# Optimization experiments

Hardware: AMD Instinct MI355X
Metric: run time of the kernel (lower is better)

The kernel has to match this reference:

```python
import jax, jax.numpy as jnp
import numpy as np

T, H, E, I = 512, 2048, 8, 1024


def setup_inputs() -> dict:
    key = jax.random.key(0)
    k1, k2, k3, k4 = jax.random.split(key, 4)
    x = jax.random.normal(k1, (T, H), dtype=jnp.float32)
    router_logits = jax.random.normal(k2, (T, E), dtype=jnp.float32)
    # w13 stacks [gate; up] along the output dim: [E, 2I, H]
    w13_weight = jax.random.normal(k3, (E, 2 * I, H), dtype=jnp.float32) * (1.0 / np.sqrt(H))
    w2_weight = jax.random.normal(k4, (E, H, I), dtype=jnp.float32) * (1.0 / np.sqrt(I))
    return {"x": x, "router_logits": router_logits, "w13_weight": w13_weight,
            "w2_weight": w2_weight, "top_k": 2}


def reference(x, router_logits, w13_weight, w2_weight, top_k):
    t, h = x.shape
    e = router_logits.shape[-1]
    # select_experts: softmax -> top_k -> renormalize
    probs = jax.nn.softmax(router_logits.astype(jnp.float32), axis=-1)  # [T, E]
    topk_w, topk_ids = jax.lax.top_k(probs, top_k)                      # [T, K]
    topk_w = topk_w / jnp.sum(topk_w, axis=-1, keepdims=True)
    # dense combine weights [T, E]; zero for unselected experts
    combine = jnp.zeros((t, e), dtype=x.dtype).at[
        jnp.arange(t)[:, None], topk_ids
    ].add(topk_w.astype(x.dtype))
    # grouped expert SwiGLU MLP (computed densely over experts, masked by combine)
    gu = jnp.einsum('th,enh->ten', x, w13_weight)   # [T, E, 2I]
    i = gu.shape[-1] // 2
    gate, up = gu[..., :i], gu[..., i:]
    act = jax.nn.silu(gate) * up                    # [T, E, I]
    y = jnp.einsum('tei,ehi->teh', act, w2_weight)  # [T, E, H]
    return jnp.einsum('teh,te->th', y, combine)     # weighted combine [T, H]
```

## Files before the change

kernel.cpp:

```cpp
#include <hip/hip_runtime.h>
#include <hip/hip_bf16.h>

#define T_TOK 512
#define H_DIM 2048
#define E_NUM 8
#define I_DIM 1024

typedef __attribute__((ext_vector_type(8))) short short8;
typedef __attribute__((ext_vector_type(4))) float f32x4;

__device__ __forceinline__ unsigned short f2bf(float f) {
    unsigned int u = __float_as_uint(f);
    u += 0x7fff + ((u >> 16) & 1);
    return (unsigned short)(u >> 16);
}

__device__ __forceinline__ short8 cvt8(float4 a, float4 b) {
    union { short8 s; __hip_bfloat162 h[4]; } u;
    u.h[0] = __float22bfloat162_rn(make_float2(a.x, a.y));
    u.h[1] = __float22bfloat162_rn(make_float2(a.z, a.w));
    u.h[2] = __float22bfloat162_rn(make_float2(b.x, b.y));
    u.h[3] = __float22bfloat162_rn(make_float2(b.z, b.w));
    return u.s;
}

__device__ __forceinline__ void gload_lds16(const void* g, void* l) {
    __builtin_amdgcn_global_load_lds(
        (const __attribute__((address_space(1))) void*)g,
        (__attribute__((address_space(3))) void*)l, 16, 0, 0);
}

__global__ __launch_bounds__(256) void xcvt_kernel(
    const float* __restrict__ x, unsigned short* __restrict__ xb)
{
    int i = (blockIdx.x * 256 + threadIdx.x) * 8;
    float4 v0 = *(const float4*)(x + i);
    float4 v1 = *(const float4*)(x + i + 4);
    *(short8*)(xb + i) = cvt8(v0, v1);
}

__global__ __launch_bounds__(512) void routing_kernel(
    const float* __restrict__ logits,
    int* __restrict__ count, int* __restrict__ bucket,
    float* __restrict__ pair_w)
{
    int t = threadIdx.x;
    if (t < E_NUM) count[t] = 0;
    __syncthreads();

    float p[E_NUM];
    float m = -INFINITY;
#pragma unroll
    for (int e = 0; e < E_NUM; ++e) {
        p[e] = logits[t * E_NUM + e];
        m = fmaxf(m, p[e]);
    }
#pragma unroll
    for (int e = 0; e < E_NUM; ++e) p[e] = expf(p[e] - m);
    int i0 = 0;
#pragma unroll
    for (int e = 1; e < E_NUM; ++e) if (p[e] > p[i0]) i0 = e;
    int i1 = (i0 == 0) ? 1 : 0;
#pragma unroll
    for (int e = 0; e < E_NUM; ++e) if (e != i0 && p[e] > p[i1]) i1 = e;
    float denom = p[i0] + p[i1];
    pair_w[2 * t + 0] = p[i0] / denom;
    pair_w[2 * t + 1] = p[i1] / denom;

    int pos0 = atomicAdd(&count[i0], 1);
    bucket[i0 * T_TOK + pos0] = 2 * t + 0;
    int pos1 = atomicAdd(&count[i1], 1);
    bucket[i1 * T_TOK + pos1] = 2 * t + 1;
}

__global__ __launch_bounds__(256) void gemm1_silu_kernel(
    const unsigned short* __restrict__ xb, const float* __restrict__ w13,
    const int* __restrict__ count, const int* __restrict__ bucket,
    __hip_bfloat16* __restrict__ act)
{
    const int e   = blockIdx.z;
    const int n_e = count[e];
    const int m0  = blockIdx.y * 64;
    if (m0 >= n_e) return;
    const int n0  = blockIdx.x * 32;

    __shared__ unsigned short sA[4][64 * 32];
    __shared__ float sG[4][32 * 32];
    __shared__ float sU[4][32 * 32];

    const int tid  = threadIdx.x;
    const int lane = tid & 63;
    const int wid  = tid >> 6;
    const int fr   = lane & 15;
    const int fq   = lane >> 4;
    const int wr   = wid >> 1;
    const int wc   = wid & 1;

    const int arow = 16 * wid + (lane >> 2);
    const int tok  = bucket[e * T_TOK + min(m0 + arow, n_e - 1)] >> 1;
    const unsigned short* aptr = xb + (size_t)tok * H_DIM + (lane & 3) * 8;
    const int grow = 8 * wid + (lane >> 3);
    const int gs   = (lane & 7) ^ (lane >> 3);
    const float* gptr = w13 + ((size_t)e * (2 * I_DIM) + n0 + grow) * H_DIM + gs * 4;
    const float* uptr = w13 + ((size_t)e * (2 * I_DIM) + I_DIM + n0 + grow) * H_DIM + gs * 4;

    auto stage = [&](int kb, int buf) {
        gload_lds16(aptr + kb, &sA[buf][16 * wid * 32]);
        gload_lds16(gptr + kb, &sG[buf][8 * wid * 32]);
        gload_lds16(uptr + kb, &sU[buf][8 * wid * 32]);
    };

    f32x4 accg[2] = {};
    f32x4 accu[2] = {};

    stage(0, 0); stage(32, 1); stage(64, 2);

    for (int t = 0; t < 64; ++t) {
        stage(min((t + 3) * 32, 2016), (t + 3) & 3);
        asm volatile("s_waitcnt vmcnt(9)" ::: "memory");
        __builtin_amdgcn_s_barrier();

        const int buf = t & 3;
        short8 a[2], bg, bu;
#pragma unroll
        for (int m = 0; m < 2; ++m)
            a[m] = *(const short8*)&sA[buf][(wr * 32 + m * 16 + fr) * 32 + fq * 8];
        {
            int r  = wc * 16 + fr;
            int s0 = (fq * 2) ^ (r & 7);
            const float* gb = &sG[buf][r * 32];
            bg = cvt8(*(const float4*)(gb + s0 * 4), *(const float4*)(gb + (s0 ^ 1) * 4));
            const float* ub = &sU[buf][r * 32];
            bu = cvt8(*(const float4*)(ub + s0 * 4), *(const float4*)(ub + (s0 ^ 1) * 4));
        }
        asm volatile("s_waitcnt lgkmcnt(0)" ::: "memory");
        __builtin_amdgcn_s_barrier();

        accg[0] = __builtin_amdgcn_mfma_f32_16x16x32_bf16(a[0], bg, accg[0], 0, 0, 0);
        accg[1] = __builtin_amdgcn_mfma_f32_16x16x32_bf16(a[1], bg, accg[1], 0, 0, 0);
        accu[0] = __builtin_amdgcn_mfma_f32_16x16x32_bf16(a[0], bu, accu[0], 0, 0, 0);
        accu[1] = __builtin_amdgcn_mfma_f32_16x16x32_bf16(a[1], bu, accu[1], 0, 0, 0);
    }
    asm volatile("s_waitcnt vmcnt(0)" ::: "memory");

#pragma unroll
    for (int m = 0; m < 2; ++m) {
#pragma unroll
        for (int j = 0; j < 4; ++j) {
            int r = m0 + wr * 32 + m * 16 + fq * 4 + j;
            if (r < n_e) {
                int pid = bucket[e * T_TOK + r];
                float g = accg[m][j];
                float u = accu[m][j];
                float sg = g / (1.f + expf(-g));
                int col = n0 + wc * 16 + fr;
                *(unsigned short*)(act + (size_t)pid * I_DIM + col) = f2bf(sg * u);
            }
        }
    }
}

__global__ __launch_bounds__(256) void gemm2_kernel(
    const __hip_bfloat16* __restrict__ act, const float* __restrict__ w2,
    const int* __restrict__ count, const int* __restrict__ bucket,
    float* __restrict__ y)
{
    const int e   = blockIdx.z;
    const int n_e = count[e];
    const int m0  = blockIdx.y * 64;
    if (m0 >= n_e) return;
    const int h0  = blockIdx.x * 32;

    __shared__ unsigned short sA[4][64 * 64];
    __shared__ float sB[4][32 * 64];

    const int tid  = threadIdx.x;
    const int lane = tid & 63;
    const int wid  = tid >> 6;
    const int fr   = lane & 15;
    const int fq   = lane >> 4;
    const int wr   = wid >> 1;
    const int wc   = wid & 1;

    const unsigned short* aptr[2];
#pragma unroll
    for (int i = 0; i < 2; ++i) {
        int r   = 16 * wid + 8 * i + (lane >> 3);
        int gsl = (lane & 7) ^ (r & 7);
        int pid = bucket[e * T_TOK + min(m0 + r, n_e - 1)];
        aptr[i] = (const unsigned short*)act + (size_t)pid * I_DIM + gsl * 8;
    }
    const float* bptr[2];
#pragma unroll
    for (int i = 0; i < 2; ++i) {
        int r   = 8 * wid + 4 * i + (lane >> 4);
        int gsl = (lane & 15) ^ (r & 7);
        bptr[i] = w2 + ((size_t)e * H_DIM + h0 + r) * I_DIM + gsl * 4;
    }

    auto stage = [&](int kb, int buf) {
#pragma unroll
        for (int i = 0; i < 2; ++i)
            gload_lds16(aptr[i] + kb, &sA[buf][(16 * wid + 8 * i) * 64]);
#pragma unroll
        for (int i = 0; i < 2; ++i)
            gload_lds16(bptr[i] + kb, &sB[buf][(8 * wid + 4 * i) * 64]);
    };

    f32x4 acc[2] = {};

    stage(0, 0); stage(64, 1); stage(128, 2);

    for (int t = 0; t < 16; ++t) {
        stage(min((t + 3) * 64, 960), (t + 3) & 3);
        asm volatile("s_waitcnt vmcnt(12)" ::: "memory");
        __builtin_amdgcn_s_barrier();

        const int buf = t & 3;
        short8 a[2][2], b[2];
#pragma unroll
        for (int kk = 0; kk < 2; ++kk) {
#pragma unroll
            for (int m = 0; m < 2; ++m) {
                int r    = wr * 32 + m * 16 + fr;
                int slot = (kk * 4 + fq) ^ (r & 7);
                a[kk][m] = *(const short8*)&sA[buf][r * 64 + slot * 8];
            }
            {
                int r  = wc * 16 + fr;
                int s0 = (kk * 8 + fq * 2) ^ (r & 7);
                const float* bb = &sB[buf][r * 64];
                b[kk] = cvt8(*(const float4*)(bb + s0 * 4), *(const float4*)(bb + (s0 ^ 1) * 4));
            }
        }
        asm volatile("s_waitcnt lgkmcnt(0)" ::: "memory");
        __builtin_amdgcn_s_barrier();

#pragma unroll
        for (int kk = 0; kk < 2; ++kk)
#pragma unroll
            for (int m = 0; m < 2; ++m)
                acc[m] = __builtin_amdgcn_mfma_f32_16x16x32_bf16(a[kk][m], b[kk], acc[m], 0, 0, 0);
    }
    asm volatile("s_waitcnt vmcnt(0)" ::: "memory");

#pragma unroll
    for (int m = 0; m < 2; ++m) {
#pragma unroll
        for (int j = 0; j < 4; ++j) {
            int r = m0 + wr * 32 + m * 16 + fq * 4 + j;
            if (r < n_e) {
                int pid = bucket[e * T_TOK + r];
                y[(size_t)pid * H_DIM + h0 + wc * 16 + fr] = acc[m][j];
            }
        }
    }
}

__global__ __launch_bounds__(256) void combine_kernel(
    const float* __restrict__ y, const float* __restrict__ pair_w,
    float* __restrict__ out)
{
    int idx = blockIdx.x * 256 + threadIdx.x;
    int t = idx >> 9;
    int c = idx & 511;
    float w0 = pair_w[2 * t + 0];
    float w1 = pair_w[2 * t + 1];
    float4 y0 = ((const float4*)(y + (size_t)(2 * t + 0) * H_DIM))[c];
    float4 y1 = ((const float4*)(y + (size_t)(2 * t + 1) * H_DIM))[c];
    float4 o;
    o.x = w0 * y0.x + w1 * y1.x;
    o.y = w0 * y0.y + w1 * y1.y;
    o.z = w0 * y0.z + w1 * y1.z;
    o.w = w0 * y0.w + w1 * y1.w;
    ((float4*)(out + (size_t)t * H_DIM))[c] = o;
}

extern "C" void kernel_launch(void* const* d_in, const int* in_sizes, int n_in,
                              void* d_out, int out_size, void* d_ws, size_t ws_size,
                              hipStream_t stream) {
    const float* x      = (const float*)d_in[0];
    const float* logits = (const float*)d_in[1];
    const float* w13    = (const float*)d_in[2];
    const float* w2     = (const float*)d_in[3];
    float* out = (float*)d_out;

    int*   count  = (int*)d_ws;
    int*   bucket = count + E_NUM;
    float* pair_w = (float*)(bucket + E_NUM * T_TOK);
    unsigned short* xb = (unsigned short*)(pair_w + 2 * T_TOK);
    __hip_bfloat16* act = (__hip_bfloat16*)(xb + (size_t)T_TOK * H_DIM);
    float* ybuf   = (float*)((unsigned short*)act + (size_t)2 * T_TOK * I_DIM);

    xcvt_kernel<<<(T_TOK * H_DIM / 8) / 256, 256, 0, stream>>>(x, xb);
    routing_kernel<<<1, 512, 0, stream>>>(logits, count, bucket, pair_w);
    gemm1_silu_kernel<<<dim3(I_DIM / 32, T_TOK / 64, E_NUM), 256, 0, stream>>>(
        xb, w13, count, bucket, act);
    gemm2_kernel<<<dim3(H_DIM / 32, T_TOK / 64, E_NUM), 256, 0, stream>>>(
        act, w2, count, bucket, ybuf);
    combine_kernel<<<(T_TOK * (H_DIM / 4)) / 256, 256, 0, stream>>>(
        ybuf, pair_w, out);
}
```

Before: 101.8 us.

## Enlarge gemm1 tile to 128 rows and 64-wide K step with 512 threads

The gate/up GEMM now uses 8 waves per block, a 128-row M tile and a 64-element K step, with a doubled inner loop over two K sub-slices. Each block covers more of an expert's tokens, so the fp32 w13 weights are fetched by fewer M blocks and there are half as many barrier rounds along K. The cost is about 128KB of LDS per block, which limits occupancy to one block per CU, and more early-exiting blocks in the grid. The gemm2 prefetch clamp is rewritten in an equivalent form.

Result: slower. 126.6 us (+24.3%).

```diff
diff --git a/kernel.cpp b/kernel.cpp
--- a/kernel.cpp
+++ b/kernel.cpp
@@ -73,20 +73,20 @@
     bucket[i1 * T_TOK + pos1] = 2 * t + 1;
 }
 
-__global__ __launch_bounds__(256) void gemm1_silu_kernel(
+__global__ __launch_bounds__(512) void gemm1_silu_kernel(
     const unsigned short* __restrict__ xb, const float* __restrict__ w13,
     const int* __restrict__ count, const int* __restrict__ bucket,
     __hip_bfloat16* __restrict__ act)
 {
     const int e   = blockIdx.z;
     const int n_e = count[e];
-    const int m0  = blockIdx.y * 64;
+    const int m0  = blockIdx.y * 128;
     if (m0 >= n_e) return;
     const int n0  = blockIdx.x * 32;
 
-    __shared__ unsigned short sA[4][64 * 32];
-    __shared__ float sG[4][32 * 32];
-    __shared__ float sU[4][32 * 32];
+    __shared__ unsigned short sA[4][128 * 64];
+    __shared__ float sG[4][32 * 64];
+    __shared__ float sU[4][32 * 64];
 
     const int tid  = threadIdx.x;
     const int lane = tid & 63;
@@ -96,50 +96,67 @@
     const int wr   = wid >> 1;
     const int wc   = wid & 1;
 
-    const int arow = 16 * wid + (lane >> 2);
-    const int tok  = bucket[e * T_TOK + min(m0 + arow, n_e - 1)] >> 1;
-    const unsigned short* aptr = xb + (size_t)tok * H_DIM + (lane & 3) * 8;
-    const int grow = 8 * wid + (lane >> 3);
-    const int gs   = (lane & 7) ^ (lane >> 3);
-    const float* gptr = w13 + ((size_t)e * (2 * I_DIM) + n0 + grow) * H_DIM + gs * 4;
-    const float* uptr = w13 + ((size_t)e * (2 * I_DIM) + I_DIM + n0 + grow) * H_DIM + gs * 4;
+    const unsigned short* aptr[2];
+#pragma unroll
+    for (int i = 0; i < 2; ++i) {
+        int r   = 8 * (2 * wid + i) + (lane >> 3);
+        int g   = (lane & 7) ^ (lane >> 3);
+        int tok = bucket[e * T_TOK + min(m0 + r, n_e - 1)] >> 1;
+        aptr[i] = xb + (size_t)tok * H_DIM + g * 8;
+    }
+    const int rG = 4 * wid + (lane >> 4);
+    const int gG = (lane & 15) ^ (rG & 7);
+    const float* gptr = w13 + ((size_t)e * (2 * I_DIM) + n0 + rG) * H_DIM + gG * 4;
+    const float* uptr = w13 + ((size_t)e * (2 * I_DIM) + I_DIM + n0 + rG) * H_DIM + gG * 4;
 
     auto stage = [&](int kb, int buf) {
-        gload_lds16(aptr + kb, &sA[buf][16 * wid * 32]);
-        gload_lds16(gptr + kb, &sG[buf][8 * wid * 32]);
-        gload_lds16(uptr + kb, &sU[buf][8 * wid * 32]);
+        gload_lds16(aptr[0] + kb, &sA[buf][(16 * wid) * 64]);
+        gload_lds16(aptr[1] + kb, &sA[buf][(16 * wid + 8) * 64]);
+        gload_lds16(gptr + kb, &sG[buf][(4 * wid) * 64]);
+        gload_lds16(uptr + kb, &sU[buf][(4 * wid) * 64]);
     };
 
     f32x4 accg[2] = {};
     f32x4 accu[2] = {};
 
-    stage(0, 0); stage(32, 1); stage(64, 2);
-
-    for (int t = 0; t < 64; ++t) {
-        stage(min((t + 3) * 32, 2016), (t + 3) & 3);
-        asm volatile("s_waitcnt vmcnt(9)" ::: "memory");
+    stage(0, 0); stage(64, 1); stage(128, 2);
+
+    for (int t = 0; t < 32; ++t) {
+        stage(min(t + 3, 31) * 64, (t + 3) & 3);
+        asm volatile("s_waitcnt vmcnt(12)" ::: "memory");
         __builtin_amdgcn_s_barrier();
 
         const int buf = t & 3;
-        short8 a[2], bg, bu;
-#pragma unroll
-        for (int m = 0; m < 2; ++m)
-            a[m] = *(const short8*)&sA[buf][(wr * 32 + m * 16 + fr) * 32 + fq * 8];
-        {
-            int r  = wc * 16 + fr;
-            int s0 = (fq * 2) ^ (r & 7);
-            const float* gb = &sG[buf][r * 32];
-            bg = cvt8(*(const float4*)(gb + s0 * 4), *(const float4*)(gb + (s0 ^ 1) * 4));
-            const float* ub = &sU[buf][r * 32];
-            bu = cvt8(*(const float4*)(ub + s0 * 4), *(const float4*)(ub + (s0 ^ 1) * 4));
+        short8 a[2][2], bg[2], bu[2];
+#pragma unroll
+        for (int kk = 0; kk < 2; ++kk) {
+#pragma unroll
+            for (int m = 0; m < 2; ++m) {
+                int r    = wr * 32 + m * 16 + fr;
+                int slot = (kk * 4 + fq) ^ (r & 7);
+                a[kk][m] = *(const short8*)&sA[buf][r * 64 + slot * 8];
+            }
+            {
+                int r  = wc * 16 + fr;
+                int s0 = (kk * 8 + fq * 2) ^ (r & 7);
+                const float* gb = &sG[buf][r * 64];
+                bg[kk] = cvt8(*(const float4*)(gb + s0 * 4),
+                              *(const float4*)(gb + (s0 ^ 1) * 4));
+                const float* ub = &sU[buf][r * 64];
+                bu[kk] = cvt8(*(const float4*)(ub + s0 * 4),
+                              *(const float4*)(ub + (s0 ^ 1) * 4));
+            }
         }
         asm volatile("s_waitcnt lgkmcnt(0)" ::: "memory");
         __builtin_amdgcn_s_barrier();
 
-        accg[0] = __builtin_amdgcn_mfma_f32_16x16x32_bf16(a[0], bg, accg[0], 0, 0, 0);
-        accg[1] = __builtin_amdgcn_mfma_f32_16x16x32_bf16(a[1], bg, accg[1], 0, 0, 0);
-        accu[0] = __builtin_amdgcn_mfma_f32_16x16x32_bf16(a[0], bu, accu[0], 0, 0, 0);
-        accu[1] = __builtin_amdgcn_mfma_f32_16x16x32_bf16(a[1], bu, accu[1], 0, 0, 0);
+#pragma unroll
+        for (int kk = 0; kk < 2; ++kk)
+#pragma unroll
+            for (int m = 0; m < 2; ++m) {
+                accg[m] = __builtin_amdgcn_mfma_f32_16x16x32_bf16(a[kk][m], bg[kk], accg[m], 0, 0, 0);
+                accu[m] = __builtin_amdgcn_mfma_f32_16x16x32_bf16(a[kk][m], bu[kk], accu[m], 0, 0, 0);
+            }
     }
     asm volatile("s_waitcnt vmcnt(0)" ::: "memory");
 
@@ -212,7 +229,7 @@
     stage(0, 0); stage(64, 1); stage(128, 2);
 
     for (int t = 0; t < 16; ++t) {
-        stage(min((t + 3) * 64, 960), (t + 3) & 3);
+        stage(min(t + 3, 15) * 64, (t + 3) & 3);
         asm volatile("s_waitcnt vmcnt(12)" ::: "memory");
         __builtin_amdgcn_s_barrier();
 
@@ -294,7 +311,7 @@
 
     xcvt_kernel<<<(T_TOK * H_DIM / 8) / 256, 256, 0, stream>>>(x, xb);
     routing_kernel<<<1, 512, 0, stream>>>(logits, count, bucket, pair_w);
-    gemm1_silu_kernel<<<dim3(I_DIM / 32, T_TOK / 64, E_NUM), 256, 0, stream>>>(
+    gemm1_silu_kernel<<<dim3(I_DIM / 32, T_TOK * 2 / 128, E_NUM), 512, 0, stream>>>(
         xb, w13, count, bucket, act);
     gemm2_kernel<<<dim3(H_DIM / 32, T_TOK / 64, E_NUM), 256, 0, stream>>>(
         act, w2, count, bucket, ybuf);
```

## Restructure MoE GEMMs: A fragments from global, bf16 weights in LDS, 128-row tiles

Applied to the files above, without the earlier changes.

Both expert GEMMs are rewritten. Activation fragments are now loaded straight from global memory into registers, and only the fp32 weights are staged through LDS. The weights are converted to bf16 once at staging time, into a swizzled double buffer with a 256-wide K step. Tiles become 128 rows by 16 columns with each wave owning 32 rows, which replaces the async global_load_lds 4-stage pipeline. The aim is to remove the repeated per-wave fp32->bf16 conversion, cut barriers per K, and raise MFMA work per synchronization, at the cost of uncoalesced register loads for A and higher register pressure.

Result: slower. 146.0 us (+43.4%).

```diff
diff --git a/kernel.cpp b/kernel.cpp
--- a/kernel.cpp
+++ b/kernel.cpp
@@ -24,12 +24,6 @@
     return u.s;
 }
 
-__device__ __forceinline__ void gload_lds16(const void* g, void* l) {
-    __builtin_amdgcn_global_load_lds(
-        (const __attribute__((address_space(1))) void*)g,
-        (__attribute__((address_space(3))) void*)l, 16, 0, 0);
-}
-
 __global__ __launch_bounds__(256) void xcvt_kernel(
     const float* __restrict__ x, unsigned short* __restrict__ xb)
 {
@@ -80,81 +74,104 @@
 {
     const int e   = blockIdx.z;
     const int n_e = count[e];
-    const int m0  = blockIdx.y * 64;
+    const int m0  = blockIdx.y * 128;
     if (m0 >= n_e) return;
-    const int n0  = blockIdx.x * 32;
-
-    __shared__ unsigned short sA[4][64 * 32];
-    __shared__ float sG[4][32 * 32];
-    __shared__ float sU[4][32 * 32];
+    const int n0  = blockIdx.x * 16;
+
+    __shared__ unsigned short sG[2][16 * 256];
+    __shared__ unsigned short sU[2][16 * 256];
 
     const int tid  = threadIdx.x;
     const int lane = tid & 63;
     const int wid  = tid >> 6;
     const int fr   = lane & 15;
     const int fq   = lane >> 4;
-    const int wr   = wid >> 1;
-    const int wc   = wid & 1;
-
-    const int arow = 16 * wid + (lane >> 2);
-    const int tok  = bucket[e * T_TOK + min(m0 + arow, n_e - 1)] >> 1;
-    const unsigned short* aptr = xb + (size_t)tok * H_DIM + (lane & 3) * 8;
-    const int grow = 8 * wid + (lane >> 3);
-    const int gs   = (lane & 7) ^ (lane >> 3);
-    const float* gptr = w13 + ((size_t)e * (2 * I_DIM) + n0 + grow) * H_DIM + gs * 4;
-    const float* uptr = w13 + ((size_t)e * (2 * I_DIM) + I_DIM + n0 + grow) * H_DIM + gs * 4;
-
-    auto stage = [&](int kb, int buf) {
-        gload_lds16(aptr + kb, &sA[buf][16 * wid * 32]);
-        gload_lds16(gptr + kb, &sG[buf][8 * wid * 32]);
-        gload_lds16(uptr + kb, &sU[buf][8 * wid * 32]);
-    };
+
+    const int srow = 4 * wid + (lane >> 4);
+    const int scol = (lane & 15) * 16;
+    const float* gsrc = w13 + ((size_t)e * 2048 + n0 + srow) * H_DIM + scol;
+    const float* usrc = w13 + ((size_t)e * 2048 + I_DIM + n0 + srow) * H_DIM + scol;
+    const int wg0 = (2 * (lane & 15) + 0) ^ (srow & 7);
+    const int wg1 = (2 * (lane & 15) + 1) ^ (srow & 7);
+
+    const unsigned short* ar[2];
+#pragma unroll
+    for (int m = 0; m < 2; ++m) {
+        int r   = m0 + wid * 32 + m * 16 + fr;
+        int tok = bucket[e * T_TOK + min(r, n_e - 1)] >> 1;
+        ar[m] = xb + (size_t)tok * H_DIM + fq * 8;
+    }
 
     f32x4 accg[2] = {};
     f32x4 accu[2] = {};
 
-    stage(0, 0); stage(32, 1); stage(64, 2);
-
-    for (int t = 0; t < 64; ++t) {
-        stage(min((t + 3) * 32, 2016), (t + 3) & 3);
-        asm volatile("s_waitcnt vmcnt(9)" ::: "memory");
-        __builtin_amdgcn_s_barrier();
-
-        const int buf = t & 3;
-        short8 a[2], bg, bu;
-#pragma unroll
-        for (int m = 0; m < 2; ++m)
-            a[m] = *(const short8*)&sA[buf][(wr * 32 + m * 16 + fr) * 32 + fq * 8];
-        {
-            int r  = wc * 16 + fr;
-            int s0 = (fq * 2) ^ (r & 7);
-            const float* gb = &sG[buf][r * 32];
-            bg = cvt8(*(const float4*)(gb + s0 * 4), *(const float4*)(gb + (s0 ^ 1) * 4));
-            const float* ub = &sU[buf][r * 32];
-            bu = cvt8(*(const float4*)(ub + s0 * 4), *(const float4*)(ub + (s0 ^ 1) * 4));
+    {
+        float4 g0 = *(const float4*)(gsrc + 0),  g1 = *(const float4*)(gsrc + 4);
+        float4 g2 = *(const float4*)(gsrc + 8),  g3 = *(const float4*)(gsrc + 12);
+        float4 u0 = *(const float4*)(usrc + 0),  u1 = *(const float4*)(usrc + 4);
+        float4 u2 = *(const float4*)(usrc + 8),  u3 = *(const float4*)(usrc + 12);
+        *(short8*)&sG[0][srow * 256 + wg0 * 8] = cvt8(g0, g1);
+        *(short8*)&sG[0][srow * 256 + wg1 * 8] = cvt8(g2, g3);
+        *(short8*)&sU[0][srow * 256 + wg0 * 8] = cvt8(u0, u1);
+        *(short8*)&sU[0][srow * 256 + wg1 * 8] = cvt8(u2, u3);
+    }
+    __syncthreads();
+
+    for (int t = 0; t < 8; ++t) {
+        const int kb      = t * 256;
+        const int kb_next = min(t + 1, 7) * 256;
+
+        short8 a[8][2];
+#pragma unroll
+        for (int kk = 0; kk < 8; ++kk)
+#pragma unroll
+            for (int m = 0; m < 2; ++m)
+                a[kk][m] = *(const short8*)(ar[m] + kb + kk * 32);
+
+        float4 g0 = *(const float4*)(gsrc + kb_next + 0);
+        float4 g1 = *(const float4*)(gsrc + kb_next + 4);
+        float4 g2 = *(const float4*)(gsrc + kb_next + 8);
+        float4 g3 = *(const float4*)(gsrc + kb_next + 12);
+        float4 u0 = *(const float4*)(usrc + kb_next + 0);
+        float4 u1 = *(const float4*)(usrc + kb_next + 4);
+        float4 u2 = *(const float4*)(usrc + kb_next + 8);
+        float4 u3 = *(const float4*)(usrc + kb_next + 12);
+
+        const unsigned short* G = sG[t & 1];
+        const unsigned short* U = sU[t & 1];
+#pragma unroll
+        for (int kk = 0; kk < 8; ++kk) {
+            int slot = (kk * 4 + fq) ^ (fr & 7);
+            short8 bg = *(const short8*)&G[fr * 256 + slot * 8];
+            short8 bu = *(const short8*)&U[fr * 256 + slot * 8];
+#pragma unroll
+            for (int m = 0; m < 2; ++m) {
+                accg[m] = __builtin_amdgcn_mfma_f32_16x16x32_bf16(a[kk][m], bg, accg[m], 0, 0, 0);
+                accu[m] = __builtin_amdgcn_mfma_f32_16x16x32_bf16(a[kk][m], bu, accu[m], 0, 0, 0);
+            }
         }
-        asm volatile("s_waitcnt lgkmcnt(0)" ::: "memory");
-        __builtin_amdgcn_s_barrier();
-
-        accg[0] = __builtin_amdgcn_mfma_f32_16x16x32_bf16(a[0], bg, accg[0], 0, 0, 0);
-        accg[1] = __builtin_amdgcn_mfma_f32_16x16x32_bf16(a[1], bg, accg[1], 0, 0, 0);
-        accu[0] = __builtin_amdgcn_mfma_f32_16x16x32_bf16(a[0], bu, accu[0], 0, 0, 0);
-        accu[1] = __builtin_amdgcn_mfma_f32_16x16x32_bf16(a[1], bu, accu[1], 0, 0, 0);
-    }
-    asm volatile("s_waitcnt vmcnt(0)" ::: "memory");
+
+        unsigned short* Gw = (unsigned short*)sG[(t + 1) & 1];
+        unsigned short* Uw = (unsigned short*)sU[(t + 1) & 1];
+        *(short8*)&Gw[srow * 256 + wg0 * 8] = cvt8(g0, g1);
+        *(short8*)&Gw[srow * 256 + wg1 * 8] = cvt8(g2, g3);
+        *(short8*)&Uw[srow * 256 + wg0 * 8] = cvt8(u0, u1);
+        *(short8*)&Uw[srow * 256 + wg1 * 8] = cvt8(u2, u3);
+
+        __syncthreads();
+    }
 
 #pragma unroll
     for (int m = 0; m < 2; ++m) {
 #pragma unroll
         for (int j = 0; j < 4; ++j) {
-            int r = m0 + wr * 32 + m * 16 + fq * 4 + j;
+            int r = m0 + wid * 32 + m * 16 + fq * 4 + j;
             if (r < n_e) {
                 int pid = bucket[e * T_TOK + r];
                 float g = accg[m][j];
                 float u = accu[m][j];
                 float sg = g / (1.f + expf(-g));
-                int col = n0 + wc * 16 + fr;
-                *(unsigned short*)(act + (size_t)pid * I_DIM + col) = f2bf(sg * u);
+                *(unsigned short*)(act + (size_t)pid * I_DIM + n0 + fr) = f2bf(sg * u);
             }
         }
     }
@@ -167,91 +184,83 @@
 {
     const int e   = blockIdx.z;
     const int n_e = count[e];
-    const int m0  = blockIdx.y * 64;
+    const int m0  = blockIdx.y * 128;
     if (m0 >= n_e) return;
-    const int h0  = blockIdx.x * 32;
-
-    __shared__ unsigned short sA[4][64 * 64];
-    __shared__ float sB[4][32 * 64];
+    const int h0  = blockIdx.x * 16;
+
+    __shared__ unsigned short sB[2][16 * 256];
 
     const int tid  = threadIdx.x;
     const int lane = tid & 63;
     const int wid  = tid >> 6;
     const int fr   = lane & 15;
     const int fq   = lane >> 4;
-    const int wr   = wid >> 1;
-    const int wc   = wid & 1;
-
-    const unsigned short* aptr[2];
-#pragma unroll
-    for (int i = 0; i < 2; ++i) {
-        int r   = 16 * wid + 8 * i + (lane >> 3);
-        int gsl = (lane & 7) ^ (r & 7);
-        int pid = bucket[e * T_TOK + min(m0 + r, n_e - 1)];
-        aptr[i] = (const unsigned short*)act + (size_t)pid * I_DIM + gsl * 8;
-    }
-    const float* bptr[2];
-#pragma unroll
-    for (int i = 0; i < 2; ++i) {
-        int r   = 8 * wid + 4 * i + (lane >> 4);
-        int gsl = (lane & 15) ^ (r & 7);
-        bptr[i] = w2 + ((size_t)e * H_DIM + h0 + r) * I_DIM + gsl * 4;
-    }
-
-    auto stage = [&](int kb, int buf) {
-#pragma unroll
-        for (int i = 0; i < 2; ++i)
-            gload_lds16(aptr[i] + kb, &sA[buf][(16 * wid + 8 * i) * 64]);
-#pragma unroll
-        for (int i = 0; i < 2; ++i)
-            gload_lds16(bptr[i] + kb, &sB[buf][(8 * wid + 4 * i) * 64]);
-    };
+
+    const int srow = 4 * wid + (lane >> 4);
+    const int scol = (lane & 15) * 16;
+    const float* bsrc = w2 + ((size_t)e * H_DIM + h0 + srow) * I_DIM + scol;
+    const int wg0 = (2 * (lane & 15) + 0) ^ (srow & 7);
+    const int wg1 = (2 * (lane & 15) + 1) ^ (srow & 7);
+
+    const unsigned short* ar[2];
+#pragma unroll
+    for (int m = 0; m < 2; ++m) {
+        int r   = m0 + wid * 32 + m * 16 + fr;
+        int pid = bucket[e * T_TOK + min(r, n_e - 1)];
+        ar[m] = (const unsigned short*)act + (size_t)pid * I_DIM + fq * 8;
+    }
 
     f32x4 acc[2] = {};
 
-    stage(0, 0); stage(64, 1); stage(128, 2);
-
-    for (int t = 0; t < 16; ++t) {
-        stage(min((t + 3) * 64, 960), (t + 3) & 3);
-        asm volatile("s_waitcnt vmcnt(12)" ::: "memory");
-        __builtin_amdgcn_s_barrier();
-
-        const int buf = t & 3;
-        short8 a[2][2], b[2];
-#pragma unroll
-        for (int kk = 0; kk < 2; ++kk) {
-#pragma unroll
-            for (int m = 0; m < 2; ++m) {
-                int r    = wr * 32 + m * 16 + fr;
-                int slot = (kk * 4 + fq) ^ (r & 7);
-                a[kk][m] = *(const short8*)&sA[buf][r * 64 + slot * 8];
-            }
-            {
-                int r  = wc * 16 + fr;
-                int s0 = (kk * 8 + fq * 2) ^ (r & 7);
-                const float* bb = &sB[buf][r * 64];
-                b[kk] = cvt8(*(const float4*)(bb + s0 * 4), *(const float4*)(bb + (s0 ^ 1) * 4));
-            }
+    {
+        float4 b0 = *(const float4*)(bsrc + 0),  b1 = *(const float4*)(bsrc + 4);
+        float4 b2 = *(const float4*)(bsrc + 8),  b3 = *(const float4*)(bsrc + 12);
+        *(short8*)&sB[0][srow * 256 + wg0 * 8] = cvt8(b0, b1);
+        *(short8*)&sB[0][srow * 256 + wg1 * 8] = cvt8(b2, b3);
+    }
+    __syncthreads();
+
+    for (int t = 0; t < 4; ++t) {
+        const int kb      = t * 256;
+        const int kb_next = min(t + 1, 3) * 256;
+
+        short8 a[8][2];
+#pragma unroll
+        for (int kk = 0; kk < 8; ++kk)
+#pragma unroll
+            for (int m = 0; m < 2; ++m)
+                a[kk][m] = *(const short8*)(ar[m] + kb + kk * 32);
+
+        float4 b0 = *(const float4*)(bsrc + kb_next + 0);
+        float4 b1 = *(const float4*)(bsrc + kb_next + 4);
+        float4 b2 = *(const float4*)(bsrc + kb_next + 8);
+        float4 b3 = *(const float4*)(bsrc + kb_next + 12);
+
+        const unsigned short* B = sB[t & 1];
+#pragma unroll
+        for (int kk = 0; kk < 8; ++kk) {
+            int slot = (kk * 4 + fq) ^ (fr & 7);
+            short8 bb = *(const short8*)&B[fr * 256 + slot * 8];
+#pragma unroll
+            for (int m = 0; m < 2; ++m)
+                acc[m] = __builtin_amdgcn_mfma_f32_16x16x32_bf16(a[kk][m], bb, acc[m], 0, 0, 0);
         }
-        asm volatile("s_waitcnt lgkmcnt(0)" ::: "memory");
-        __builtin_amdgcn_s_barrier();
-
-#pragma unroll
-        for (int kk = 0; kk < 2; ++kk)
-#pragma unroll
-            for (int m = 0; m < 2; ++m)
-                acc[m] = __builtin_amdgcn_mfma_f32_16x16x32_bf16(a[kk][m], b[kk], acc[m], 0, 0, 0);
-    }
-    asm volatile("s_waitcnt vmcnt(0)" ::: "memory");
+
+        unsigned short* Bw = (unsigned short*)sB[(t + 1) & 1];
+        *(short8*)&Bw[srow * 256 + wg0 * 8] = cvt8(b0, b1);
+        *(short8*)&Bw[srow * 256 + wg1 * 8] = cvt8(b2, b3);
+
+        __syncthreads();
+    }
 
 #pragma unroll
     for (int m = 0; m < 2; ++m) {
 #pragma unroll
         for (int j = 0; j < 4; ++j) {
-            int r = m0 + wr * 32 + m * 16 + fq * 4 + j;
+            int r = m0 + wid * 32 + m * 16 + fq * 4 + j;
             if (r < n_e) {
                 int pid = bucket[e * T_TOK + r];
-                y[(size_t)pid * H_DIM + h0 + wc * 16 + fr] = acc[m][j];
+                y[(size_t)pid * H_DIM + h0 + fr] = acc[m][j];
             }
         }
     }
@@ -294,9 +303,9 @@
 
     xcvt_kernel<<<(T_TOK * H_DIM / 8) / 256, 256, 0, stream>>>(x, xb);
     routing_kernel<<<1, 512, 0, stream>>>(logits, count, bucket, pair_w);
-    gemm1_silu_kernel<<<dim3(I_DIM / 32, T_TOK / 64, E_NUM), 256, 0, stream>>>(
+    gemm1_silu_kernel<<<dim3(I_DIM / 16, 4, E_NUM), 256, 0, stream>>>(
         xb, w13, count, bucket, act);
-    gemm2_kernel<<<dim3(H_DIM / 32, T_TOK / 64, E_NUM), 256, 0, stream>>>(
+    gemm2_kernel<<<dim3(H_DIM / 16, 4, E_NUM), 256, 0, stream>>>(
         act, w2, count, bucket, ybuf);
     combine_kernel<<<(T_TOK * (H_DIM / 4)) / 256, 256, 0, stream>>>(
         ybuf, pair_w, out);
```
